# Kernel tuning notes

Measured on AMD Instinct MI355X. Metric: run time of the kernel, lower is better.

Reference implementation:

```python
import jax, jax.numpy as jnp
import numpy as np

D_MODEL = 1024
D_INNER = 2048
D_STATE = 16
D_CONV = 4
DT_RANK = 64
BATCH = 2
SEQLEN = 1024


def setup_inputs() -> dict:
    key = jax.random.key(0)
    ks = jax.random.split(key, 12)
    s = 0.02
    # dt bias initialized as inverse-softplus of dt ~ LogUniform(1e-3, 1e-1), as in the torch code
    dt = jnp.exp(jax.random.uniform(ks[7], (D_INNER,)) * (np.log(0.1) - np.log(0.001)) + np.log(0.001))
    dt = jnp.clip(dt, 1e-4, None)
    inv_dt = jnp.log(jnp.expm1(dt))
    A_log = jnp.log(jnp.broadcast_to(jnp.arange(1, D_STATE + 1, dtype=jnp.float32), (D_INNER, D_STATE)))
    return {
        "hidden_states": jax.random.normal(ks[0], (BATCH, SEQLEN, D_MODEL), jnp.float32),
        "x_text": jax.random.normal(ks[1], (BATCH, D_MODEL), jnp.float32),
        "in_proj_w": jax.random.normal(ks[2], (2 * D_INNER, D_MODEL), jnp.float32) * s,
        "conv_w": jax.random.normal(ks[3], (D_INNER, 1, D_CONV), jnp.float32) * s,
        "conv_b": jax.random.normal(ks[4], (D_INNER,), jnp.float32) * s,
        "x_proj_w": jax.random.normal(ks[5], (DT_RANK + 2 * D_STATE, D_INNER), jnp.float32) * s,
        "dt_proj_w": jax.random.normal(ks[6], (D_INNER, DT_RANK), jnp.float32) * (DT_RANK ** -0.5),
        "dt_proj_b": inv_dt.astype(jnp.float32),
        "A_log": A_log.astype(jnp.float32),
        "D": jnp.ones((D_INNER,), jnp.float32),
        "out_proj_w": jax.random.normal(ks[8], (D_MODEL, D_INNER), jnp.float32) * s,
        "gate_w": jax.random.normal(ks[9], (DT_RANK + 2 * D_STATE, D_MODEL), jnp.float32) * s,
        "gate_b": jnp.zeros((DT_RANK + 2 * D_STATE,), jnp.float32),
    }


def _causal_depthwise_conv(x, w, b):
    # x: (b, d, l), w: (d, 1, k) depthwise, left-pad k-1 for causality
    y = jax.lax.conv_general_dilated(
        x, w, window_strides=(1,), padding=[(D_CONV - 1, 0)],
        dimension_numbers=("NCH", "OIH", "NCH"), feature_group_count=D_INNER)
    return y + b[None, :, None]


def _mamba_forward(hidden_states, x_text, in_proj_w, conv_w, conv_b, x_proj_w,
                   dt_proj_w, dt_proj_b, A_log, D, out_proj_w, gate_w, gate_b):
    b = hidden_states.shape[0]
    # input projection -> x, z each (b, l, d_inner)
    xz = jnp.einsum("bld,ed->ble", hidden_states, in_proj_w)
    x, z = jnp.split(xz, 2, axis=-1)
    # causal depthwise conv + SiLU
    xc = _causal_depthwise_conv(jnp.transpose(x, (0, 2, 1)), conv_w, conv_b)
    xc = jnp.transpose(jax.nn.silu(xc), (0, 2, 1))  # (b, l, d_inner)
    # x_proj -> dt/B/C, modulated by text gate
    x_dbl = jnp.einsum("bld,ed->ble", xc, x_proj_w)  # (b, l, dt_rank+2n)
    gate = jax.nn.sigmoid(x_text @ gate_w.T + gate_b)  # (b, dt_rank+2n)
    x_dbl = x_dbl * gate[:, None, :]
    dt, Bm, Cm = jnp.split(x_dbl, [DT_RANK, DT_RANK + D_STATE], axis=-1)
    delta = jax.nn.softplus(jnp.einsum("blr,dr->bld", dt, dt_proj_w) + dt_proj_b)  # (b, l, d)
    A = -jnp.exp(A_log)  # (d, n)
    dA = jnp.exp(jnp.einsum("bld,dn->bldn", delta, A))          # (b, l, d, n)
    dBx = jnp.einsum("bld,bln->bldn", delta * xc, Bm)            # (b, l, d, n)

    def step(h, inp):
        dA_t, dBx_t, C_t = inp
        h = h * dA_t + dBx_t                       # (b, d, n)
        y_t = jnp.einsum("bdn,bn->bd", h, C_t)
        return h, y_t

    h0 = jnp.zeros((b, D_INNER, D_STATE), delta.dtype)
    _, ys = jax.lax.scan(step, h0, (jnp.transpose(dA, (1, 0, 2, 3)),
                                    jnp.transpose(dBx, (1, 0, 2, 3)),
                                    jnp.transpose(Cm, (1, 0, 2))))
    y = jnp.transpose(ys, (1, 0, 2)) + D * xc      # (b, l, d_inner)
    y = y * jax.nn.silu(z)
    return jnp.einsum("bld,md->blm", y, out_proj_w)


def reference(hidden_states, x_text, in_proj_w, conv_w, conv_b, x_proj_w,
              dt_proj_w, dt_proj_b, A_log, D, out_proj_w, gate_w, gate_b):
    return _mamba_forward(hidden_states, x_text, in_proj_w, conv_w, conv_b, x_proj_w,
                          dt_proj_w, dt_proj_b, A_log, D, out_proj_w, gate_w, gate_b)
```

## Files before the change

kernel.cpp:

```cpp
#include <hip/hip_runtime.h>

#define BATCH   2
#define SEQLEN  1024
#define DMODEL  1024
#define DINNER  2048
#define DSTATE  16
#define DCONV   4
#define DTRANK  64
#define GDIM    96
#define MROWS   (BATCH*SEQLEN)

#define NCHUNK  64
#define LCHUNK  16
#define SPLITX  32

typedef __attribute__((ext_vector_type(8))) short bf16x8_t;
typedef __attribute__((ext_vector_type(4))) float f32x4_t;
typedef __attribute__((ext_vector_type(4))) unsigned short u16x4_t;
typedef unsigned short ushort_t;

__device__ __forceinline__ unsigned short f2bf(float x) {
    union { float f; unsigned int u; } v; v.f = x;
    unsigned int r = v.u + 0x7FFFu + ((v.u >> 16) & 1u);
    return (unsigned short)(r >> 16);
}
__device__ __forceinline__ float bf2f(unsigned short h) {
    union { unsigned int u; float f; } v; v.u = ((unsigned int)h) << 16;
    return v.f;
}

__device__ __forceinline__ void gload_lds16(const ushort_t* g, short* l) {
    __builtin_amdgcn_global_load_lds(
        (const __attribute__((address_space(1))) unsigned int*)g,
        (__attribute__((address_space(3))) unsigned int*)l, 16, 0, 0);
}

#define N1 (MROWS*DMODEL)
#define N2 (2*DINNER*DMODEL)
#define N3 (GDIM*DINNER)
#define N4 (DINNER*DTRANK)
#define N5 (DMODEL*DINNER)
#define NTOT (N1+N2+N3+N4+N5)
#define CVTN (NTOT/4)
#define Z1   (MROWS*DMODEL/4)
#define Z2   (MROWS*GDIM/4)
#define CVTBLK ((CVTN + Z1 + Z2) / 256)
__global__ __launch_bounds__(256)
void cvt5z_kernel(const float* __restrict__ s1, const float* __restrict__ s2,
                  const float* __restrict__ s3, const float* __restrict__ s4,
                  const float* __restrict__ s5,
                  ushort_t* o1, ushort_t* o2, ushort_t* o3, ushort_t* o4, ushort_t* o5,
                  float* __restrict__ z1, float* __restrict__ z2) {
    int t = blockIdx.x * 256 + threadIdx.x;
    if (t < CVTN) {
        int idx = t * 4;
        const float* src; ushort_t* dst;
        if (idx < N1)              { src = s1; dst = o1; }
        else if ((idx -= N1) < N2) { src = s2; dst = o2; }
        else if ((idx -= N2) < N3) { src = s3; dst = o3; }
        else if ((idx -= N3) < N4) { src = s4; dst = o4; }
        else                       { idx -= N4; src = s5; dst = o5; }
        f32x4_t v = *(const f32x4_t*)(src + idx);
        u16x4_t o;
        #pragma unroll
        for (int j = 0; j < 4; j++) o[j] = f2bf(v[j]);
        *(u16x4_t*)(dst + idx) = o;
    } else if ((t -= CVTN) < Z1) {
        ((f32x4_t*)z1)[t] = (f32x4_t){0.f, 0.f, 0.f, 0.f};
    } else {
        t -= Z1;
        ((f32x4_t*)z2)[t] = (f32x4_t){0.f, 0.f, 0.f, 0.f};
    }
}

template<int EPI>
__global__ __launch_bounds__(256)
void gemm_bf(const ushort_t* __restrict__ A, const ushort_t* __restrict__ W,
             void* __restrict__ out0, void* __restrict__ out1,
             const float* __restrict__ bias, int M, int N, int K) {
    __shared__ __align__(16) short As[2][128 * 32];
    __shared__ __align__(16) short Bs[2][128 * 32];

    const int tid  = threadIdx.x;
    const int m0   = blockIdx.x * 128;
    const int n0   = blockIdx.y * 128;
    const int klen = K / gridDim.z;
    const int kbeg = blockIdx.z * klen;

    const int w    = tid >> 6;
    const int lane = tid & 63;
    const int quad = lane >> 4;
    const int l15  = lane & 15;
    const int wm   = (w >> 1) * 64;
    const int wn   = (w & 1) * 64;

    const int rA0 = (w * 2 + 0) * 16 + (lane >> 2);
    const int rA1 = (w * 2 + 1) * 16 + (lane >> 2);
    const int kc  = (((lane & 3) ^ ((lane >> 2) & 3)) << 3);
    const int arow0 = m0 + rA0;
    const int arow1 = m0 + rA1;
    int brow0 = n0 + rA0; if (brow0 > N - 1) brow0 = N - 1;
    int brow1 = n0 + rA1; if (brow1 > N - 1) brow1 = N - 1;

    f32x4_t acc[4][4];
    #pragma unroll
    for (int i = 0; i < 4; i++)
        #pragma unroll
        for (int j = 0; j < 4; j++)
            acc[i][j] = (f32x4_t){0.f, 0.f, 0.f, 0.f};

    {
        const int kk = kbeg + kc;
        gload_lds16(A + (size_t)arow0 * K + kk, &As[0][(w * 2 + 0) * 512]);
        gload_lds16(A + (size_t)arow1 * K + kk, &As[0][(w * 2 + 1) * 512]);
        gload_lds16(W + (size_t)brow0 * K + kk, &Bs[0][(w * 2 + 0) * 512]);
        gload_lds16(W + (size_t)brow1 * K + kk, &Bs[0][(w * 2 + 1) * 512]);
    }
    __syncthreads();

    int cur = 0;
    for (int k0 = 0; k0 < klen; k0 += 32) {
        if (k0 + 32 < klen) {
            const int kk = kbeg + k0 + 32 + kc;
            gload_lds16(A + (size_t)arow0 * K + kk, &As[cur ^ 1][(w * 2 + 0) * 512]);
            gload_lds16(A + (size_t)arow1 * K + kk, &As[cur ^ 1][(w * 2 + 1) * 512]);
            gload_lds16(W + (size_t)brow0 * K + kk, &Bs[cur ^ 1][(w * 2 + 0) * 512]);
            gload_lds16(W + (size_t)brow1 * K + kk, &Bs[cur ^ 1][(w * 2 + 1) * 512]);
        }
        bf16x8_t af[4], bfv[4];
        #pragma unroll
        for (int mi = 0; mi < 4; mi++) {
            int row = wm + mi * 16 + l15;
            af[mi] = *(const bf16x8_t*)(&As[cur][row * 32 + ((quad ^ (row & 3)) << 3)]);
        }
        #pragma unroll
        for (int ni = 0; ni < 4; ni++) {
            int row = wn + ni * 16 + l15;
            bfv[ni] = *(const bf16x8_t*)(&Bs[cur][row * 32 + ((quad ^ (row & 3)) << 3)]);
        }
        #pragma unroll
        for (int mi = 0; mi < 4; mi++)
            #pragma unroll
            for (int ni = 0; ni < 4; ni++)
                acc[mi][ni] = __builtin_amdgcn_mfma_f32_16x16x32_bf16(af[mi], bfv[ni], acc[mi][ni], 0, 0, 0);
        __syncthreads();
        cur ^= 1;
    }

    #pragma unroll
    for (int mi = 0; mi < 4; mi++) {
        #pragma unroll
        for (int ni = 0; ni < 4; ni++) {
            #pragma unroll
            for (int r = 0; r < 4; r++) {
                int gm = m0 + wm + mi * 16 + quad * 4 + r;
                int gn = n0 + wn + ni * 16 + l15;
                if (gn < N) {
                    float v = acc[mi][ni][r];
                    if (EPI == 1) {
                        float t = v + bias[gn];
                        float sp = (t > 20.f) ? t : log1pf(__expf(t));
                        ((ushort_t*)out0)[(size_t)gm * N + gn] = f2bf(sp);
                    } else if (EPI == 3) {
                        if (gn < DINNER)
                            ((float*)out0)[(size_t)gm * DINNER + gn] = v;
                        else
                            ((float*)out1)[(size_t)gm * DINNER + (gn - DINNER)] = v;
                    } else {
                        atomicAdd(&((float*)out0)[(size_t)gm * N + gn], v);
                    }
                }
            }
        }
    }
}

#define CONVBLK ((MROWS*DINNER)/256)
__global__ __launch_bounds__(256)
void convgate_kernel(const float* __restrict__ x,
                     const float* __restrict__ cw,
                     const float* __restrict__ cb,
                     ushort_t* __restrict__ xc,
                     const float* __restrict__ xt,
                     const float* __restrict__ gw,
                     const float* __restrict__ gb,
                     float* __restrict__ gate) {
    if (blockIdx.x < CONVBLK) {
        int idx = blockIdx.x * 256 + threadIdx.x;
        int d  = idx & (DINNER - 1);
        int bl = idx >> 11;
        int l  = bl & (SEQLEN - 1);
        float acc = cb[d];
        #pragma unroll
        for (int j = 0; j < DCONV; j++) {
            int lj = l - (DCONV - 1) + j;
            if (lj >= 0)
                acc += cw[d * DCONV + j] * x[(size_t)(bl - (DCONV - 1) + j) * DINNER + d];
        }
        float v = acc / (1.f + __expf(-acc));
        xc[idx] = f2bf(v);
    } else {
        int g = blockIdx.x - CONVBLK;
        int b = g / GDIM, j = g % GDIM;
        int tid = threadIdx.x;
        float s = 0.f;
        for (int k = tid; k < DMODEL; k += 256)
            s += xt[b * DMODEL + k] * gw[j * DMODEL + k];
        #pragma unroll
        for (int o = 32; o > 0; o >>= 1) s += __shfl_down(s, o);
        __shared__ float red[4];
        if ((tid & 63) == 0) red[tid >> 6] = s;
        __syncthreads();
        if (tid == 0) {
            float t = red[0] + red[1] + red[2] + red[3] + gb[j];
            gate[b * GDIM + j] = 1.f / (1.f + __expf(-t));
        }
    }
}

__global__ void gatemul_kernel(const float* __restrict__ xp,
                               const float* __restrict__ gate,
                               ushort_t* __restrict__ dt,
                               float* __restrict__ Bm,
                               float* __restrict__ Cm) {
    int idx = blockIdx.x * 256 + threadIdx.x;
    if (idx >= MROWS * GDIM) return;
    int j  = idx % GDIM;
    int bl = idx / GDIM;
    int b  = bl >> 10;
    float v = xp[idx] * gate[b * GDIM + j];
    if (j < DTRANK)               dt[bl * DTRANK + j] = f2bf(v);
    else if (j < DTRANK + DSTATE) Bm[bl * DSTATE + (j - DTRANK)] = v;
    else                          Cm[bl * DSTATE + (j - DTRANK - DSTATE)] = v;
}

__global__ __launch_bounds__(256)
void scan1_kernel(const ushort_t* __restrict__ delta,
                  const ushort_t* __restrict__ xc,
                  const float* __restrict__ Bm,
                  const float* __restrict__ A_log,
                  float* __restrict__ hfin,
                  float* __restrict__ dsum) {
    __shared__ float sBm[LCHUNK][DSTATE];
    int tid = threadIdx.x;
    int d = blockIdx.x * 256 + tid;
    int b = blockIdx.y;
    int c = blockIdx.z;
    int l0 = c * LCHUNK;
    for (int t = tid; t < LCHUNK * DSTATE; t += 256)
        sBm[t >> 4][t & 15] = Bm[((size_t)(b * SEQLEN + l0 + (t >> 4))) * DSTATE + (t & 15)];
    __syncthreads();

    float Ac[DSTATE];
    #pragma unroll
    for (int n = 0; n < DSTATE; n++)
        Ac[n] = -__expf(A_log[d * DSTATE + n]);
    float h[DSTATE];
    #pragma unroll
    for (int n = 0; n < DSTATE; n++) h[n] = 0.f;
    float ds = 0.f;

    for (int s = 0; s < LCHUNK; s++) {
        size_t ix = (size_t)(b * SEQLEN + l0 + s) * DINNER + d;
        float dv = bf2f(delta[ix]);
        float xv = bf2f(xc[ix]);
        float dx = dv * xv;
        ds += dv;
        #pragma unroll
        for (int n = 0; n < DSTATE; n++) {
            float e = __expf(dv * Ac[n]);
            h[n] = h[n] * e + dx * sBm[s][n];
        }
    }
    size_t base = ((size_t)(b * DINNER + d) * NCHUNK + c) * DSTATE;
    #pragma unroll
    for (int n = 0; n < DSTATE; n++) hfin[base + n] = h[n];
    dsum[((size_t)b * NCHUNK + c) * DINNER + d] = ds;
}

__global__ __launch_bounds__(256)
void scan2_kernel(float* __restrict__ hfin,
                  const float* __restrict__ dsum,
                  const float* __restrict__ A_log) {
    __shared__ float sh[NCHUNK * DSTATE];
    __shared__ float sp[NCHUNK * DSTATE];
    __shared__ float sAc[DSTATE];
    __shared__ float sds[NCHUNK];
    const int tid = threadIdx.x;
    const int bd  = blockIdx.x;
    const int b   = bd >> 11;
    const int d   = bd & (DINNER - 1);
    if (tid < DSTATE) sAc[tid] = -__expf(A_log[d * DSTATE + tid]);
    if (tid < NCHUNK) sds[tid] = dsum[((size_t)b * NCHUNK + tid) * DINNER + d];
    const size_t base = (size_t)bd * (NCHUNK * DSTATE);
    float hl[4];
    #pragma unroll
    for (int r = 0; r < 4; r++) hl[r] = hfin[base + tid + r * 256];
    __syncthreads();
    #pragma unroll
    for (int r = 0; r < 4; r++) {
        int i = tid + r * 256;
        sh[i] = hl[r];
        sp[i] = __expf(sAc[i & 15] * sds[i >> 4]);
    }
    __syncthreads();
    #pragma unroll
    for (int s = 1; s < NCHUNK; s <<= 1) {
        float nh[4], np[4];
        #pragma unroll
        for (int r = 0; r < 4; r++) {
            int i = tid + r * 256;
            int c = i >> 4;
            if (c >= s) {
                int j = i - (s << 4);
                nh[r] = sh[i] + sp[i] * sh[j];
                np[r] = sp[i] * sp[j];
            } else { nh[r] = sh[i]; np[r] = sp[i]; }
        }
        __syncthreads();
        #pragma unroll
        for (int r = 0; r < 4; r++) { int i = tid + r * 256; sh[i] = nh[r]; sp[i] = np[r]; }
        __syncthreads();
    }
    #pragma unroll
    for (int r = 0; r < 4; r++) {
        int i = tid + r * 256;
        hfin[base + i] = (i >> 4) ? sh[i - 16] : 0.f;
    }
}

__global__ __launch_bounds__(256)
void scan3_kernel(const ushort_t* __restrict__ delta,
                  ushort_t* __restrict__ xc,
                  const float* __restrict__ z,
                  const float* __restrict__ Bm,
                  const float* __restrict__ Cm,
                  const float* __restrict__ A_log,
                  const float* __restrict__ Dp,
                  const float* __restrict__ h0) {
    __shared__ float sBm[LCHUNK][DSTATE];
    __shared__ float sCm[LCHUNK][DSTATE];
    int tid = threadIdx.x;
    int d = blockIdx.x * 256 + tid;
    int b = blockIdx.y;
    int c = blockIdx.z;
    int l0 = c * LCHUNK;
    for (int t = tid; t < LCHUNK * DSTATE; t += 256) {
        size_t src = ((size_t)(b * SEQLEN + l0 + (t >> 4))) * DSTATE + (t & 15);
        sBm[t >> 4][t & 15] = Bm[src];
        sCm[t >> 4][t & 15] = Cm[src];
    }
    __syncthreads();

    float Ac[DSTATE];
    #pragma unroll
    for (int n = 0; n < DSTATE; n++)
        Ac[n] = -__expf(A_log[d * DSTATE + n]);

    float h[DSTATE];
    size_t hb0 = ((size_t)(b * DINNER + d) * NCHUNK + c) * DSTATE;
    #pragma unroll
    for (int n = 0; n < DSTATE; n++) h[n] = h0[hb0 + n];

    float Dv = Dp[d];

    for (int s = 0; s < LCHUNK; s++) {
        size_t ix = (size_t)(b * SEQLEN + l0 + s) * DINNER + d;
        float dv = bf2f(delta[ix]);
        float xv = bf2f(xc[ix]);
        float dx = dv * xv;
        float y = 0.f;
        #pragma unroll
        for (int n = 0; n < DSTATE; n++) {
            float e = __expf(dv * Ac[n]);
            h[n] = h[n] * e + dx * sBm[s][n];
            y += h[n] * sCm[s][n];
        }
        float zv = z[ix];
        float o = (y + Dv * xv) * (zv / (1.f + __expf(-zv)));
        xc[ix] = f2bf(o);
    }
}

extern "C" void kernel_launch(void* const* d_in, const int* in_sizes, int n_in,
                              void* d_out, int out_size, void* d_ws, size_t ws_size,
                              hipStream_t stream) {
    const float* hidden   = (const float*)d_in[0];
    const float* x_text   = (const float*)d_in[1];
    const float* in_proj  = (const float*)d_in[2];
    const float* conv_w   = (const float*)d_in[3];
    const float* conv_b   = (const float*)d_in[4];
    const float* x_proj   = (const float*)d_in[5];
    const float* dt_proj  = (const float*)d_in[6];
    const float* dt_bias  = (const float*)d_in[7];
    const float* A_log    = (const float*)d_in[8];
    const float* Dparam   = (const float*)d_in[9];
    const float* out_proj = (const float*)d_in[10];
    const float* gate_w   = (const float*)d_in[11];
    const float* gate_b   = (const float*)d_in[12];

    char* ws = (char*)d_ws;
    size_t off = 0;
    auto alloc = [&](size_t bytes) -> char* {
        char* p = ws + off;
        off += (bytes + 255) & ~(size_t)255;
        return p;
    };
    ushort_t* hb    = (ushort_t*)alloc((size_t)N1 * 2);
    ushort_t* w_in  = (ushort_t*)alloc((size_t)N2 * 2);
    ushort_t* w_x   = (ushort_t*)alloc((size_t)N3 * 2);
    ushort_t* w_dt  = (ushort_t*)alloc((size_t)N4 * 2);
    ushort_t* w_o   = (ushort_t*)alloc((size_t)N5 * 2);
    float*    X     = (float*)alloc((size_t)MROWS * DINNER * 4);
    float*    zbuf  = (float*)alloc((size_t)MROWS * DINNER * 4);
    float*    hfin  = (float*)alloc((size_t)BATCH * DINNER * NCHUNK * DSTATE * 4);
    float*    dsum  = (float*)alloc((size_t)BATCH * NCHUNK * DINNER * 4);
    float*    xdbl  = (float*)alloc((size_t)MROWS * GDIM * 4);
    float*    gate  = (float*)alloc((size_t)BATCH * GDIM * 4);
    float*    Bm    = (float*)alloc((size_t)MROWS * DSTATE * 4);
    float*    Cm    = (float*)alloc((size_t)MROWS * DSTATE * 4);
    ushort_t* dt    = (ushort_t*)alloc((size_t)MROWS * DTRANK * 2);

    ushort_t* xc    = w_in;
    ushort_t* delta = (ushort_t*)X;

    cvt5z_kernel<<<CVTBLK, 256, 0, stream>>>(
        hidden, in_proj, x_proj, dt_proj, out_proj, hb, w_in, w_x, w_dt, w_o,
        (float*)d_out, xdbl);

    gemm_bf<3><<<dim3(MROWS / 128, (2 * DINNER) / 128, 1), 256, 0, stream>>>(
        hb, w_in, X, zbuf, nullptr, MROWS, 2 * DINNER, DMODEL);

    convgate_kernel<<<CONVBLK + BATCH * GDIM, 256, 0, stream>>>(
        X, conv_w, conv_b, xc, x_text, gate_w, gate_b, gate);

    gemm_bf<4><<<dim3(MROWS / 128, 1, SPLITX), 256, 0, stream>>>(
        xc, w_x, xdbl, nullptr, nullptr, MROWS, GDIM, DINNER);

    gatemul_kernel<<<(MROWS * GDIM + 255) / 256, 256, 0, stream>>>(
        xdbl, gate, dt, Bm, Cm);

    gemm_bf<1><<<dim3(MROWS / 128, DINNER / 128, 1), 256, 0, stream>>>(
        dt, w_dt, delta, nullptr, dt_bias, MROWS, DINNER, DTRANK);

    scan1_kernel<<<dim3(DINNER / 256, BATCH, NCHUNK), 256, 0, stream>>>(
        delta, xc, Bm, A_log, hfin, dsum);

    scan2_kernel<<<BATCH * DINNER, 256, 0, stream>>>(hfin, dsum, A_log);

    scan3_kernel<<<dim3(DINNER / 256, BATCH, NCHUNK), 256, 0, stream>>>(
        delta, xc, zbuf, Bm, Cm, A_log, Dparam, hfin);

    gemm_bf<4><<<dim3(MROWS / 128, DMODEL / 128, 4), 256, 0, stream>>>(
        xc, w_o, (float*)d_out, nullptr, nullptr, MROWS, DMODEL, DINNER);
}
```

Before: 308.9 us.

## Replace split-K atomics with partial buffers and explicit reductions; fix LDS swizzle

The split-K GEMMs now write per-split partial results to workspace buffers instead of using float atomicAdd. The x_proj partials are summed inside gatemul and the out_proj partials by a new reduce4 kernel. Because nothing accumulates into zeroed memory anymore, the zero-fill in the conversion kernel is removed. The LDS swizzle pattern also changes to XOR with (row>>1)&3 rather than row&3, meant to cut bank conflicts on the fragment reads. The cost is extra partial-buffer traffic (32 splits for x_proj) and one additional kernel launch.

```diff
diff --git a/kernel.cpp b/kernel.cpp
--- a/kernel.cpp
+++ b/kernel.cpp
@@ -41,36 +41,24 @@
 #define N4 (DINNER*DTRANK)
 #define N5 (DMODEL*DINNER)
 #define NTOT (N1+N2+N3+N4+N5)
-#define CVTN (NTOT/4)
-#define Z1   (MROWS*DMODEL/4)
-#define Z2   (MROWS*GDIM/4)
-#define CVTBLK ((CVTN + Z1 + Z2) / 256)
-__global__ __launch_bounds__(256)
-void cvt5z_kernel(const float* __restrict__ s1, const float* __restrict__ s2,
-                  const float* __restrict__ s3, const float* __restrict__ s4,
-                  const float* __restrict__ s5,
-                  ushort_t* o1, ushort_t* o2, ushort_t* o3, ushort_t* o4, ushort_t* o5,
-                  float* __restrict__ z1, float* __restrict__ z2) {
-    int t = blockIdx.x * 256 + threadIdx.x;
-    if (t < CVTN) {
-        int idx = t * 4;
-        const float* src; ushort_t* dst;
-        if (idx < N1)              { src = s1; dst = o1; }
-        else if ((idx -= N1) < N2) { src = s2; dst = o2; }
-        else if ((idx -= N2) < N3) { src = s3; dst = o3; }
-        else if ((idx -= N3) < N4) { src = s4; dst = o4; }
-        else                       { idx -= N4; src = s5; dst = o5; }
-        f32x4_t v = *(const f32x4_t*)(src + idx);
-        u16x4_t o;
-        #pragma unroll
-        for (int j = 0; j < 4; j++) o[j] = f2bf(v[j]);
-        *(u16x4_t*)(dst + idx) = o;
-    } else if ((t -= CVTN) < Z1) {
-        ((f32x4_t*)z1)[t] = (f32x4_t){0.f, 0.f, 0.f, 0.f};
-    } else {
-        t -= Z1;
-        ((f32x4_t*)z2)[t] = (f32x4_t){0.f, 0.f, 0.f, 0.f};
-    }
+__global__ __launch_bounds__(256)
+void cvt5_kernel(const float* __restrict__ s1, const float* __restrict__ s2,
+                 const float* __restrict__ s3, const float* __restrict__ s4,
+                 const float* __restrict__ s5,
+                 ushort_t* o1, ushort_t* o2, ushort_t* o3, ushort_t* o4, ushort_t* o5) {
+    int idx = (blockIdx.x * 256 + threadIdx.x) * 4;
+    if (idx >= NTOT) return;
+    const float* src; ushort_t* dst;
+    if (idx < N1)              { src = s1; dst = o1; }
+    else if ((idx -= N1) < N2) { src = s2; dst = o2; }
+    else if ((idx -= N2) < N3) { src = s3; dst = o3; }
+    else if ((idx -= N3) < N4) { src = s4; dst = o4; }
+    else                       { idx -= N4; src = s5; dst = o5; }
+    f32x4_t v = *(const f32x4_t*)(src + idx);
+    u16x4_t o;
+    #pragma unroll
+    for (int j = 0; j < 4; j++) o[j] = f2bf(v[j]);
+    *(u16x4_t*)(dst + idx) = o;
 }
 
 template<int EPI>
@@ -96,11 +84,13 @@
 
     const int rA0 = (w * 2 + 0) * 16 + (lane >> 2);
     const int rA1 = (w * 2 + 1) * 16 + (lane >> 2);
-    const int kc  = (((lane & 3) ^ ((lane >> 2) & 3)) << 3);
+    const int kc  = (((lane & 3) ^ ((lane >> 3) & 3)) << 3);
     const int arow0 = m0 + rA0;
     const int arow1 = m0 + rA1;
     int brow0 = n0 + rA0; if (brow0 > N - 1) brow0 = N - 1;
     int brow1 = n0 + rA1; if (brow1 > N - 1) brow1 = N - 1;
+
+    const int sw = ((quad ^ ((l15 >> 1) & 3)) << 3);
 
     f32x4_t acc[4][4];
     #pragma unroll
@@ -129,15 +119,11 @@
         }
         bf16x8_t af[4], bfv[4];
         #pragma unroll
-        for (int mi = 0; mi < 4; mi++) {
-            int row = wm + mi * 16 + l15;
-            af[mi] = *(const bf16x8_t*)(&As[cur][row * 32 + ((quad ^ (row & 3)) << 3)]);
-        }
-        #pragma unroll
-        for (int ni = 0; ni < 4; ni++) {
-            int row = wn + ni * 16 + l15;
-            bfv[ni] = *(const bf16x8_t*)(&Bs[cur][row * 32 + ((quad ^ (row & 3)) << 3)]);
-        }
+        for (int mi = 0; mi < 4; mi++)
+            af[mi] = *(const bf16x8_t*)(&As[cur][(wm + mi * 16 + l15) * 32 + sw]);
+        #pragma unroll
+        for (int ni = 0; ni < 4; ni++)
+            bfv[ni] = *(const bf16x8_t*)(&Bs[cur][(wn + ni * 16 + l15) * 32 + sw]);
         #pragma unroll
         for (int mi = 0; mi < 4; mi++)
             #pragma unroll
@@ -147,6 +133,7 @@
         cur ^= 1;
     }
 
+    const size_t zoff = (size_t)blockIdx.z * M * N;
     #pragma unroll
     for (int mi = 0; mi < 4; mi++) {
         #pragma unroll
@@ -157,17 +144,17 @@
                 int gn = n0 + wn + ni * 16 + l15;
                 if (gn < N) {
                     float v = acc[mi][ni][r];
-                    if (EPI == 1) {
+                    if (EPI == 0) {
+                        ((float*)out0)[zoff + (size_t)gm * N + gn] = v;
+                    } else if (EPI == 1) {
                         float t = v + bias[gn];
                         float sp = (t > 20.f) ? t : log1pf(__expf(t));
                         ((ushort_t*)out0)[(size_t)gm * N + gn] = f2bf(sp);
-                    } else if (EPI == 3) {
+                    } else {
                         if (gn < DINNER)
                             ((float*)out0)[(size_t)gm * DINNER + gn] = v;
                         else
                             ((float*)out1)[(size_t)gm * DINNER + (gn - DINNER)] = v;
-                    } else {
-                        atomicAdd(&((float*)out0)[(size_t)gm * N + gn], v);
                     }
                 }
             }
@@ -228,7 +215,11 @@
     int j  = idx % GDIM;
     int bl = idx / GDIM;
     int b  = bl >> 10;
-    float v = xp[idx] * gate[b * GDIM + j];
+    float v = 0.f;
+    #pragma unroll
+    for (int z = 0; z < SPLITX; z++)
+        v += xp[(size_t)z * MROWS * GDIM + idx];
+    v *= gate[b * GDIM + j];
     if (j < DTRANK)               dt[bl * DTRANK + j] = f2bf(v);
     else if (j < DTRANK + DSTATE) Bm[bl * DSTATE + (j - DTRANK)] = v;
     else                          Cm[bl * DSTATE + (j - DTRANK - DSTATE)] = v;
@@ -382,6 +373,12 @@
     }
 }
 
+__global__ void reduce4_kernel(const float* __restrict__ p, float* __restrict__ out, int n) {
+    int i = blockIdx.x * 256 + threadIdx.x;
+    if (i < n)
+        out[i] = (p[i] + p[(size_t)n + i]) + (p[2 * (size_t)n + i] + p[3 * (size_t)n + i]);
+}
+
 extern "C" void kernel_launch(void* const* d_in, const int* in_sizes, int n_in,
                               void* d_out, int out_size, void* d_ws, size_t ws_size,
                               hipStream_t stream) {
@@ -413,9 +410,8 @@
     ushort_t* w_o   = (ushort_t*)alloc((size_t)N5 * 2);
     float*    X     = (float*)alloc((size_t)MROWS * DINNER * 4);
     float*    zbuf  = (float*)alloc((size_t)MROWS * DINNER * 4);
-    float*    hfin  = (float*)alloc((size_t)BATCH * DINNER * NCHUNK * DSTATE * 4);
+    float*    xpart = (float*)alloc((size_t)SPLITX * MROWS * GDIM * 4);
     float*    dsum  = (float*)alloc((size_t)BATCH * NCHUNK * DINNER * 4);
-    float*    xdbl  = (float*)alloc((size_t)MROWS * GDIM * 4);
     float*    gate  = (float*)alloc((size_t)BATCH * GDIM * 4);
     float*    Bm    = (float*)alloc((size_t)MROWS * DSTATE * 4);
     float*    Cm    = (float*)alloc((size_t)MROWS * DSTATE * 4);
@@ -423,10 +419,11 @@
 
     ushort_t* xc    = w_in;
     ushort_t* delta = (ushort_t*)X;
-
-    cvt5z_kernel<<<CVTBLK, 256, 0, stream>>>(
-        hidden, in_proj, x_proj, dt_proj, out_proj, hb, w_in, w_x, w_dt, w_o,
-        (float*)d_out, xdbl);
+    float*    hfin  = xpart;
+    float*    outp  = X;
+
+    cvt5_kernel<<<(NTOT / 4 + 255) / 256, 256, 0, stream>>>(
+        hidden, in_proj, x_proj, dt_proj, out_proj, hb, w_in, w_x, w_dt, w_o);
 
     gemm_bf<3><<<dim3(MROWS / 128, (2 * DINNER) / 128, 1), 256, 0, stream>>>(
         hb, w_in, X, zbuf, nullptr, MROWS, 2 * DINNER, DMODEL);
@@ -434,11 +431,11 @@
     convgate_kernel<<<CONVBLK + BATCH * GDIM, 256, 0, stream>>>(
         X, conv_w, conv_b, xc, x_text, gate_w, gate_b, gate);
 
-    gemm_bf<4><<<dim3(MROWS / 128, 1, SPLITX), 256, 0, stream>>>(
-        xc, w_x, xdbl, nullptr, nullptr, MROWS, GDIM, DINNER);
+    gemm_bf<0><<<dim3(MROWS / 128, 1, SPLITX), 256, 0, stream>>>(
+        xc, w_x, xpart, nullptr, nullptr, MROWS, GDIM, DINNER);
 
     gatemul_kernel<<<(MROWS * GDIM + 255) / 256, 256, 0, stream>>>(
-        xdbl, gate, dt, Bm, Cm);
+        xpart, gate, dt, Bm, Cm);
 
     gemm_bf<1><<<dim3(MROWS / 128, DINNER / 128, 1), 256, 0, stream>>>(
         dt, w_dt, delta, nullptr, dt_bias, MROWS, DINNER, DTRANK);
@@ -451,6 +448,9 @@
     scan3_kernel<<<dim3(DINNER / 256, BATCH, NCHUNK), 256, 0, stream>>>(
         delta, xc, zbuf, Bm, Cm, A_log, Dparam, hfin);
 
-    gemm_bf<4><<<dim3(MROWS / 128, DMODEL / 128, 4), 256, 0, stream>>>(
-        xc, w_o, (float*)d_out, nullptr, nullptr, MROWS, DMODEL, DINNER);
-}
+    gemm_bf<0><<<dim3(MROWS / 128, DMODEL / 128, 4), 256, 0, stream>>>(
+        xc, w_o, outp, nullptr, nullptr, MROWS, DMODEL, DINNER);
+
+    reduce4_kernel<<<(MROWS * DMODEL + 255) / 256, 256, 0, stream>>>(
+        outp, (float*)d_out, MROWS * DMODEL);
+}
```

Result: faster. 288.2 us (-6.7%).
